# Kernel tuning notes

Hardware: AMD Instinct MI355X
Metric: run time of the kernel (lower is better)

## Reference

```python
import jax, jax.numpy as jnp
import numpy as np

HIGH_THRESHOLD = 0.1
EPS = 1e-6


def _gaussian_kernel_2d(ksize=5, sigma=1.0):
    x = np.arange(ksize, dtype=np.float32) - ksize // 2
    g = np.exp(-(x * x) / (2.0 * sigma * sigma))
    g = g / g.sum()
    return (g[:, None] * g[None, :]).astype(np.float32)  # (5,5)


def _sobel_kernels():
    gx = np.array([[-1.0, 0.0, 1.0], [-2.0, 0.0, 2.0], [-1.0, 0.0, 1.0]], np.float32)
    gy = gx.T.copy()
    return np.stack([gx, gy])[:, None]  # (2,1,3,3)


def _nms_kernels():
    # kornia get_canny_nms_kernel: 8 direction kernels, center 1, -1 at neighbor
    k = np.zeros((8, 1, 3, 3), np.float32)
    k[:, 0, 1, 1] = 1.0
    offs = [(1, 2), (0, 2), (0, 1), (0, 0), (1, 0), (2, 0), (2, 1), (2, 2)]
    for i, (r, c) in enumerate(offs):
        k[i, 0, r, c] = -1.0
    return k


def _conv(x, w, pad, mode=None):
    # x: (B,Cin,H,W), w: (Cout,Cin,kh,kw)
    if mode is not None:
        x = jnp.pad(x, ((0, 0), (0, 0), (pad, pad), (pad, pad)), mode=mode)
        padding = 'VALID'
    else:
        padding = [(pad, pad), (pad, pad)]
    return jax.lax.conv_general_dilated(
        x, w, (1, 1), padding, dimension_numbers=('NCHW', 'OIHW', 'NCHW'))


def cal_edge(x):
    dt = x.dtype
    if x.shape[1] == 3:  # rgb_to_grayscale
        w = jnp.array([0.299, 0.587, 0.114], dt).reshape(1, 3, 1, 1)
        x = jnp.sum(x * w, axis=1, keepdims=True)
    # gaussian_blur2d, reflect border (kornia default)
    blurred = _conv(x, jnp.asarray(_gaussian_kernel_2d())[None, None], 2, mode='reflect')
    # spatial_gradient (sobel, replicate border)
    grads = _conv(blurred, jnp.asarray(_sobel_kernels()), 1, mode='edge')  # (B,2,H,W)
    gx, gy = grads[:, 0:1], grads[:, 1:2]
    magnitude = jnp.sqrt(gx * gx + gy * gy + EPS)  # (B,1,H,W)
    angle = jnp.arctan2(gy, gx) * (180.0 / np.pi)
    angle = jnp.round(angle / 45.0) * 45.0
    nms_mag = _conv(magnitude, jnp.asarray(_nms_kernels()), 1)  # (B,8,H,W), zero pad
    pos_idx = jnp.mod(angle / 45.0, 8.0).astype(jnp.int32)        # (B,1,H,W)
    neg_idx = jnp.mod(angle / 45.0 + 4.0, 8.0).astype(jnp.int32)
    cp = jnp.take_along_axis(nms_mag, pos_idx, axis=1)
    cn = jnp.take_along_axis(nms_mag, neg_idx, axis=1)
    is_max = jnp.minimum(cp, cn) > 0.0
    magnitude = magnitude * is_max
    # F.threshold(mag, high, 0); then F.threshold(-e, -high, -1); e = -e
    e1 = jnp.where(magnitude > HIGH_THRESHOLD, magnitude, jnp.zeros((), dt))
    edges = -jnp.where(-e1 > -HIGH_THRESHOLD, -e1, jnp.full((), -1.0, dt))
    return edges


def setup_inputs() -> dict:
    key = jax.random.key(0)
    k1, k2 = jax.random.split(key)
    shape = (8, 3, 1024, 1024)
    op = jax.random.uniform(k1, shape, jnp.float32)
    gt = jax.random.uniform(k2, shape, jnp.float32)
    return {'op': op, 'gt': gt}


def reference(op, gt):
    edge_op = cal_edge(op)
    edge_gt = cal_edge(gt)
    return jnp.mean(jnp.abs(edge_op - edge_gt))
```

## Files before the change

### kernel.cpp

```cpp
#include <hip/hip_runtime.h>

#define N 1024
#define NN (N * N)
#define STRIPS 19
#define SEGS 32
#define SEGROWS 32
#define NWAVES (STRIPS * SEGS * 8)

__device__ __forceinline__ int refl(int i) {
    if (i < 0) return -i;
    if (i >= N) return 2 * N - 2 - i;
    return i;
}

__global__ __launch_bounds__(64)
void edge_diff_kernel(const float* __restrict__ op, const float* __restrict__ gt,
                      unsigned int* __restrict__ partials)
{
    const float w0 = 0.05448868f, w1 = 0.24420134f, w2 = 0.40261996f,
                w3 = 0.24420134f, w4 = 0.05448868f;

    int b = blockIdx.x;
    int img   = b / (STRIPS * SEGS);
    int rem   = b - img * (STRIPS * SEGS);
    int strip = rem / SEGS;
    int seg   = rem - strip * SEGS;
    int lane  = threadIdx.x;

    int cb = strip * 56 - 4;
    int c  = cb + lane;
    int cR = refl(c);

    const float* A = op + (size_t)img * 3 * NN;
    const float* B = gt + (size_t)img * 3 * NN;

    const bool cz0 = (c == 0), czN = (c == N - 1);
    const bool valid = (lane >= 4) && (lane <= 59) && (c >= 0) && (c < N);

    const int iL1 = lane - 1, iL2 = lane - 2, iR1 = lane + 1, iR2 = lane + 2;

    float ha0=0,ha1=0,ha2=0,ha3=0,ha4=0;
    float bla0=0,bla1=0,bla2=0;
    float mga0=0,mga1=0,mga2=0;
    float mgla0=0,mgla1=0,mgla2=0;
    float mgra0=0,mgra1=0,mgra2=0;
    int   axa = 0;
    float hb0=0,hb1=0,hb2=0,hb3=0,hb4=0;
    float blb0=0,blb1=0,blb2=0;
    float mgb0=0,mgb1=0,mgb2=0;
    float mglb0=0,mglb1=0,mglb2=0;
    float mgrb0=0,mgrb1=0,mgrb2=0;
    int   axb = 0;

    int acc = 0;
    const int R0 = seg * SEGROWS;

#pragma unroll 4
    for (int y = R0 - 4; y <= R0 + 35; ++y) {
        int rr = refl(y);
        const float* pa = A + (size_t)rr * N + cR;
        const float* pb = B + (size_t)rr * N + cR;

        float ga = 0.299f * pa[0] + 0.587f * pa[NN] + 0.114f * pa[2 * NN];
        float gb = 0.299f * pb[0] + 0.587f * pb[NN] + 0.114f * pb[2 * NN];

        float gal2 = __shfl(ga, iL2, 64), gal1 = __shfl(ga, iL1, 64);
        float gar1 = __shfl(ga, iR1, 64), gar2 = __shfl(ga, iR2, 64);
        float gbl2 = __shfl(gb, iL2, 64), gbl1 = __shfl(gb, iL1, 64);
        float gbr1 = __shfl(gb, iR1, 64), gbr2 = __shfl(gb, iR2, 64);
        float hna = w0*gal2 + w1*gal1 + w2*ga + w3*gar1 + w4*gar2;
        float hnb = w0*gbl2 + w1*gbl1 + w2*gb + w3*gbr1 + w4*gbr2;
        ha0=ha1; ha1=ha2; ha2=ha3; ha3=ha4; ha4=hna;
        hb0=hb1; hb1=hb2; hb2=hb3; hb3=hb4; hb4=hnb;

        float bna = w0*ha0 + w1*ha1 + w2*ha2 + w3*ha3 + w4*ha4;
        float bnb = w0*hb0 + w1*hb1 + w2*hb2 + w3*hb3 + w4*hb4;
        bla0=bla1; bla1=bla2; bla2=bna;
        blb0=blb1; blb1=blb2; blb2=bnb;

        int z = y - 3;
        float Ara = (z == 0)     ? bla1 : bla0;
        float Cra = (z == N - 1) ? bla1 : bla2;
        float Arb = (z == 0)     ? blb1 : blb0;
        float Crb = (z == N - 1) ? blb1 : blb2;

        float sa = Ara + 2.f*bla1 + Cra;  float da = Cra - Ara;
        float sb = Arb + 2.f*blb1 + Crb;  float db = Crb - Arb;

        float sal = __shfl(sa, iL1, 64), sar = __shfl(sa, iR1, 64);
        float dal = __shfl(da, iL1, 64), dar = __shfl(da, iR1, 64);
        float sbl = __shfl(sb, iL1, 64), sbr = __shfl(sb, iR1, 64);
        float dbl = __shfl(db, iL1, 64), dbr = __shfl(db, iR1, 64);
        sal = cz0 ? sa : sal;  dal = cz0 ? da : dal;
        sar = czN ? sa : sar;  dar = czN ? da : dar;
        sbl = cz0 ? sb : sbl;  dbl = cz0 ? db : dbl;
        sbr = czN ? sb : sbr;  dbr = czN ? db : dbr;

        float gxa = sar - sal;            float gya = dal + 2.f*da + dar;
        float gxb = sbr - sbl;            float gyb = dbl + 2.f*db + dbr;
        float maga = sqrtf(gxa*gxa + gya*gya + 1e-6f);
        float magb = sqrtf(gxb*gxb + gyb*gyb + 1e-6f);

        float axx = fabsf(gxa), ayy = fabsf(gya);
        int cda = (ayy <= 0.41421356f * axx) ? 0
                : (ayy >= 2.41421356f * axx) ? 1
                : (((gxa > 0.f) == (gya > 0.f)) ? 2 : 3);
        float bxx = fabsf(gxb), byy = fabsf(gyb);
        int cdb = (byy <= 0.41421356f * bxx) ? 0
                : (byy >= 2.41421356f * bxx) ? 1
                : (((gxb > 0.f) == (gyb > 0.f)) ? 2 : 3);

        float mala = __shfl(maga, iL1, 64); mala = cz0 ? 0.f : mala;
        float mara = __shfl(maga, iR1, 64); mara = czN ? 0.f : mara;
        float malb = __shfl(magb, iL1, 64); malb = cz0 ? 0.f : malb;
        float marb = __shfl(magb, iR1, 64); marb = czN ? 0.f : marb;

        mga0=mga1;   mga1=mga2;   mga2=maga;
        mgla0=mgla1; mgla1=mgla2; mgla2=mala;
        mgra0=mgra1; mgra1=mgra2; mgra2=mara;
        mgb0=mgb1;   mgb1=mgb2;   mgb2=magb;
        mglb0=mglb1; mglb1=mglb2; mglb2=malb;
        mgrb0=mgrb1; mgrb1=mgrb2; mgrb2=marb;

        int axUa = axa; axa = cda;
        int axUb = axb; axb = cdb;

        if (y >= R0 + 4) {
            int w = y - 4;
            float m0a = mga0, l0a = mgla0, r0a = mgra0;
            float m2a = mga2, l2a = mgla2, r2a = mgra2;
            float m0b = mgb0, l0b = mglb0, r0b = mgrb0;
            float m2b = mgb2, l2b = mglb2, r2b = mgrb2;
            if (w == 0)     { m0a=0; l0a=0; r0a=0; m0b=0; l0b=0; r0b=0; }
            if (w == N - 1) { m2a=0; l2a=0; r2a=0; m2b=0; l2b=0; r2b=0; }

            float n1a = (axUa == 0) ? mgra1 : (axUa == 1) ? m0a : (axUa == 2) ? r0a : l0a;
            float n2a = (axUa == 0) ? mgla1 : (axUa == 1) ? m2a : (axUa == 2) ? l2a : r2a;
            float n1b = (axUb == 0) ? mgrb1 : (axUb == 1) ? m0b : (axUb == 2) ? r0b : l0b;
            float n2b = (axUb == 0) ? mglb1 : (axUb == 1) ? m2b : (axUb == 2) ? l2b : r2b;

            bool ea = (mga1 > n1a) && (mga1 > n2a) && (mga1 > 0.1f);
            bool eb = (mgb1 > n1b) && (mgb1 > n2b) && (mgb1 > 0.1f);
            acc += (int)(valid && (ea != eb));
        }
    }

    for (int off = 32; off > 0; off >>= 1)
        acc += __shfl_down(acc, off, 64);
    if (lane == 0)
        partials[b] = (unsigned int)acc;
}

__global__ __launch_bounds__(256)
void finalize_kernel(const unsigned int* __restrict__ partials, float* __restrict__ out)
{
    __shared__ unsigned int ws[4];
    int tid = threadIdx.x;
    unsigned int sum = 0;
    for (int i = tid; i < NWAVES; i += 256)
        sum += partials[i];
    int d = (int)sum;
    for (int off = 32; off > 0; off >>= 1)
        d += __shfl_down(d, off, 64);
    if ((tid & 63) == 0) ws[tid >> 6] = (unsigned int)d;
    __syncthreads();
    if (tid == 0)
        out[0] = (float)(ws[0] + ws[1] + ws[2] + ws[3]) / 8388608.0f;
}

extern "C" void kernel_launch(void* const* d_in, const int* in_sizes, int n_in,
                              void* d_out, int out_size, void* d_ws, size_t ws_size,
                              hipStream_t stream)
{
    const float* op = (const float*)d_in[0];
    const float* gt = (const float*)d_in[1];
    unsigned int* partials = (unsigned int*)d_ws;

    edge_diff_kernel<<<dim3(NWAVES), dim3(64), 0, stream>>>(op, gt, partials);
    finalize_kernel<<<1, dim3(256), 0, stream>>>(partials, (float*)d_out);
}
```

Baseline: 232.9 us.

## Process two columns per lane with float2 loads and specialize edge strips

Each lane now handles two adjacent columns, so a wave covers 120 valid columns instead of 56. This cuts the redundant halo loads and the shuffles needed per output pixel, and interior strips use vectorized float2 loads. Border handling is moved into a templated variant that only the edge strips run. Segments are shortened to 16 rows, which gives more waves but a larger share of vertical halo rows recomputed per segment, and each lane needs more registers.

```diff
diff --git a/kernel.cpp b/kernel.cpp
--- a/kernel.cpp
+++ b/kernel.cpp
@@ -2,9 +2,9 @@
 
 #define N 1024
 #define NN (N * N)
-#define STRIPS 19
-#define SEGS 32
-#define SEGROWS 32
+#define STRIPS 9
+#define SEGS 64
+#define SEGROWS 16
 #define NWAVES (STRIPS * SEGS * 8)
 
 __device__ __forceinline__ int refl(int i) {
@@ -12,14 +12,181 @@
     if (i >= N) return 2 * N - 2 - i;
     return i;
 }
+__device__ __forceinline__ float shl(float v, int sl) { return __shfl(v, sl, 64); }
+
+struct F2 { float x, y; };
+
+__device__ __forceinline__ int axcode(float gx, float gy) {
+    float ax = fabsf(gx), ay = fabsf(gy);
+    return (ay <= 0.41421356f * ax) ? 0
+         : (ay >= 2.41421356f * ax) ? 1
+         : (((gx > 0.f) == (gy > 0.f)) ? 2 : 3);
+}
+
+__device__ __forceinline__ float pick(int code, float r, float u, float ur, float ul) {
+    return code == 0 ? r : code == 1 ? u : code == 2 ? ur : ul;
+}
+
+template<bool EC>
+__device__ __forceinline__ int strip_body(const float* __restrict__ A,
+                                          const float* __restrict__ B,
+                                          int cb, int R0, int lane)
+{
+    const float w0 = 0.05448868f, w1 = 0.24420134f, w2 = 0.40261996f,
+                w3 = 0.24420134f, w4 = 0.05448868f;
+    const int c0 = cb + 2 * lane, c1 = c0 + 1;
+    const int lm = lane - 1, lp = lane + 1;
+    const int cR0 = refl(c0), cR1 = refl(c1);
+    const bool p0 = (c0 == 0);
+    const bool pN = (c1 == N - 1);
+    const bool v0 = (lane >= 2 && lane <= 61 && c0 >= 0 && c0 < N);
+    const bool v1 = (lane >= 2 && lane <= 61 && c1 < N);
+
+    F2 ha0{},ha1{},ha2{},ha3{},ha4{}, hb0{},hb1{},hb2{},hb3{},hb4{};
+    F2 bla0{},bla1{},bla2{}, blb0{},blb1{},blb2{};
+    F2 mga0{},mga1{},mga2{}, mgla0{},mgla1{},mgla2{}, mgra0{},mgra1{},mgra2{};
+    F2 mgb0{},mgb1{},mgb2{}, mglb0{},mglb1{},mglb2{}, mgrb0{},mgrb1{},mgrb2{};
+    int axax = 0, axay = 0, axbx = 0, axby = 0;
+
+    int acc = 0;
+
+#pragma unroll 4
+    for (int y = R0 - 4; y <= R0 + SEGROWS + 3; ++y) {
+        const int rr = refl(y);
+        F2 ga, gb;
+        if (EC) {
+            const float* pa0 = A + (size_t)rr * N + cR0;
+            const float* pa1 = A + (size_t)rr * N + cR1;
+            const float* pb0 = B + (size_t)rr * N + cR0;
+            const float* pb1 = B + (size_t)rr * N + cR1;
+            ga.x = 0.299f*pa0[0] + 0.587f*pa0[NN] + 0.114f*pa0[2*NN];
+            ga.y = 0.299f*pa1[0] + 0.587f*pa1[NN] + 0.114f*pa1[2*NN];
+            gb.x = 0.299f*pb0[0] + 0.587f*pb0[NN] + 0.114f*pb0[2*NN];
+            gb.y = 0.299f*pb1[0] + 0.587f*pb1[NN] + 0.114f*pb1[2*NN];
+        } else {
+            const float* pa = A + (size_t)rr * N + c0;
+            const float* pb = B + (size_t)rr * N + c0;
+            float2 r  = *(const float2*)pa;
+            float2 g  = *(const float2*)(pa + NN);
+            float2 bb = *(const float2*)(pa + 2 * NN);
+            ga.x = 0.299f*r.x + 0.587f*g.x + 0.114f*bb.x;
+            ga.y = 0.299f*r.y + 0.587f*g.y + 0.114f*bb.y;
+            r  = *(const float2*)pb;
+            g  = *(const float2*)(pb + NN);
+            bb = *(const float2*)(pb + 2 * NN);
+            gb.x = 0.299f*r.x + 0.587f*g.x + 0.114f*bb.x;
+            gb.y = 0.299f*r.y + 0.587f*g.y + 0.114f*bb.y;
+        }
+
+        float gaLx = shl(ga.x, lm), gaLy = shl(ga.y, lm);
+        float gaRx = shl(ga.x, lp), gaRy = shl(ga.y, lp);
+        float gbLx = shl(gb.x, lm), gbLy = shl(gb.y, lm);
+        float gbRx = shl(gb.x, lp), gbRy = shl(gb.y, lp);
+        F2 hna, hnb;
+        hna.x = w0*gaLx + w1*gaLy + w2*ga.x + w3*ga.y + w4*gaRx;
+        hna.y = w0*gaLy + w1*ga.x + w2*ga.y + w3*gaRx + w4*gaRy;
+        hnb.x = w0*gbLx + w1*gbLy + w2*gb.x + w3*gb.y + w4*gbRx;
+        hnb.y = w0*gbLy + w1*gb.x + w2*gb.y + w3*gbRx + w4*gbRy;
+        ha0=ha1; ha1=ha2; ha2=ha3; ha3=ha4; ha4=hna;
+        hb0=hb1; hb1=hb2; hb2=hb3; hb3=hb4; hb4=hnb;
+
+        F2 bna, bnb;
+        bna.x = w0*ha0.x + w1*ha1.x + w2*ha2.x + w3*ha3.x + w4*ha4.x;
+        bna.y = w0*ha0.y + w1*ha1.y + w2*ha2.y + w3*ha3.y + w4*ha4.y;
+        bnb.x = w0*hb0.x + w1*hb1.x + w2*hb2.x + w3*hb3.x + w4*hb4.x;
+        bnb.y = w0*hb0.y + w1*hb1.y + w2*hb2.y + w3*hb3.y + w4*hb4.y;
+        bla0=bla1; bla1=bla2; bla2=bna;
+        blb0=blb1; blb1=blb2; blb2=bnb;
+
+        const int z = y - 3;
+        F2 bA0 = bla0, bA2 = bla2, bB0 = blb0, bB2 = blb2;
+        if (z == 0)     { bA0 = bla1; bB0 = blb1; }
+        if (z == N - 1) { bA2 = bla1; bB2 = blb1; }
+        F2 sa, da, sb, db;
+        sa.x = bA0.x + 2.f*bla1.x + bA2.x;  sa.y = bA0.y + 2.f*bla1.y + bA2.y;
+        da.x = bA2.x - bA0.x;               da.y = bA2.y - bA0.y;
+        sb.x = bB0.x + 2.f*blb1.x + bB2.x;  sb.y = bB0.y + 2.f*blb1.y + bB2.y;
+        db.x = bB2.x - bB0.x;               db.y = bB2.y - bB0.y;
+
+        float saLy = shl(sa.y, lm), saRx = shl(sa.x, lp);
+        float daLy = shl(da.y, lm), daRx = shl(da.x, lp);
+        float sbLy = shl(sb.y, lm), sbRx = shl(sb.x, lp);
+        float dbLy = shl(db.y, lm), dbRx = shl(db.x, lp);
+        if (EC) {
+            saLy = p0 ? sa.x : saLy;  daLy = p0 ? da.x : daLy;
+            sbLy = p0 ? sb.x : sbLy;  dbLy = p0 ? db.x : dbLy;
+            saRx = pN ? sa.y : saRx;  daRx = pN ? da.y : daRx;
+            sbRx = pN ? sb.y : sbRx;  dbRx = pN ? db.y : dbRx;
+        }
+        F2 gxa, gya, gxb, gyb;
+        gxa.x = sa.y - saLy;              gxa.y = saRx - sa.x;
+        gya.x = daLy + 2.f*da.x + da.y;   gya.y = da.x + 2.f*da.y + daRx;
+        gxb.x = sb.y - sbLy;              gxb.y = sbRx - sb.x;
+        gyb.x = dbLy + 2.f*db.x + db.y;   gyb.y = db.x + 2.f*db.y + dbRx;
+
+        F2 maga, magb;
+        maga.x = sqrtf(gxa.x*gxa.x + gya.x*gya.x + 1e-6f);
+        maga.y = sqrtf(gxa.y*gxa.y + gya.y*gya.y + 1e-6f);
+        magb.x = sqrtf(gxb.x*gxb.x + gyb.x*gyb.x + 1e-6f);
+        magb.y = sqrtf(gxb.y*gxb.y + gyb.y*gyb.y + 1e-6f);
+
+        int cax = axcode(gxa.x, gya.x), cay = axcode(gxa.y, gya.y);
+        int cbx = axcode(gxb.x, gyb.x), cby = axcode(gxb.y, gyb.y);
+
+        float maLy = shl(maga.y, lm), maRx = shl(maga.x, lp);
+        float mbLy = shl(magb.y, lm), mbRx = shl(magb.x, lp);
+        if (EC) {
+            maLy = p0 ? 0.f : maLy;  mbLy = p0 ? 0.f : mbLy;
+            maRx = pN ? 0.f : maRx;  mbRx = pN ? 0.f : mbRx;
+        }
+        F2 mla{maLy, maga.x}, mra{maga.y, maRx};
+        F2 mlb{mbLy, magb.x}, mrb{magb.y, mbRx};
+
+        mga0=mga1;   mga1=mga2;   mga2=maga;
+        mgla0=mgla1; mgla1=mgla2; mgla2=mla;
+        mgra0=mgra1; mgra1=mgra2; mgra2=mra;
+        mgb0=mgb1;   mgb1=mgb2;   mgb2=magb;
+        mglb0=mglb1; mglb1=mglb2; mglb2=mlb;
+        mgrb0=mgrb1; mgrb1=mgrb2; mgrb2=mrb;
+
+        const int axUax = axax, axUay = axay, axUbx = axbx, axUby = axby;
+        axax = cax; axay = cay; axbx = cbx; axby = cby;
+
+        if (y >= R0 + 4) {
+            const int w = y - 4;
+            F2 upA=mga0, upLA=mgla0, upRA=mgra0, dnA=mga2, dnLA=mgla2, dnRA=mgra2;
+            F2 upB=mgb0, upLB=mglb0, upRB=mgrb0, dnB=mgb2, dnLB=mglb2, dnRB=mgrb2;
+            if (w == 0) {
+                upA = F2{0,0}; upLA = F2{0,0}; upRA = F2{0,0};
+                upB = F2{0,0}; upLB = F2{0,0}; upRB = F2{0,0};
+            }
+            if (w == N - 1) {
+                dnA = F2{0,0}; dnLA = F2{0,0}; dnRA = F2{0,0};
+                dnB = F2{0,0}; dnLB = F2{0,0}; dnRB = F2{0,0};
+            }
+            float n1ax = pick(axUax, mgra1.x, upA.x, upRA.x, upLA.x);
+            float n2ax = pick(axUax, mgla1.x, dnA.x, dnLA.x, dnRA.x);
+            float n1ay = pick(axUay, mgra1.y, upA.y, upRA.y, upLA.y);
+            float n2ay = pick(axUay, mgla1.y, dnA.y, dnLA.y, dnRA.y);
+            float n1bx = pick(axUbx, mgrb1.x, upB.x, upRB.x, upLB.x);
+            float n2bx = pick(axUbx, mglb1.x, dnB.x, dnLB.x, dnRB.x);
+            float n1by = pick(axUby, mgrb1.y, upB.y, upRB.y, upLB.y);
+            float n2by = pick(axUby, mglb1.y, dnB.y, dnLB.y, dnRB.y);
+            bool eax = (mga1.x > n1ax) && (mga1.x > n2ax) && (mga1.x > 0.1f);
+            bool eay = (mga1.y > n1ay) && (mga1.y > n2ay) && (mga1.y > 0.1f);
+            bool ebx = (mgb1.x > n1bx) && (mgb1.x > n2bx) && (mgb1.x > 0.1f);
+            bool eby = (mgb1.y > n1by) && (mgb1.y > n2by) && (mgb1.y > 0.1f);
+            acc += (int)(v0 && (eax != ebx));
+            acc += (int)(v1 && (eay != eby));
+        }
+    }
+    return acc;
+}
 
 __global__ __launch_bounds__(64)
 void edge_diff_kernel(const float* __restrict__ op, const float* __restrict__ gt,
                       unsigned int* __restrict__ partials)
 {
-    const float w0 = 0.05448868f, w1 = 0.24420134f, w2 = 0.40261996f,
-                w3 = 0.24420134f, w4 = 0.05448868f;
-
     int b = blockIdx.x;
     int img   = b / (STRIPS * SEGS);
     int rem   = b - img * (STRIPS * SEGS);
@@ -27,128 +194,20 @@
     int seg   = rem - strip * SEGS;
     int lane  = threadIdx.x;
 
-    int cb = strip * 56 - 4;
-    int c  = cb + lane;
-    int cR = refl(c);
-
+    int cb = strip * 120 - 4;
+    int R0 = seg * SEGROWS;
     const float* A = op + (size_t)img * 3 * NN;
     const float* B = gt + (size_t)img * 3 * NN;
 
-    const bool cz0 = (c == 0), czN = (c == N - 1);
-    const bool valid = (lane >= 4) && (lane <= 59) && (c >= 0) && (c < N);
-
-    const int iL1 = lane - 1, iL2 = lane - 2, iR1 = lane + 1, iR2 = lane + 2;
-
-    float ha0=0,ha1=0,ha2=0,ha3=0,ha4=0;
-    float bla0=0,bla1=0,bla2=0;
-    float mga0=0,mga1=0,mga2=0;
-    float mgla0=0,mgla1=0,mgla2=0;
-    float mgra0=0,mgra1=0,mgra2=0;
-    int   axa = 0;
-    float hb0=0,hb1=0,hb2=0,hb3=0,hb4=0;
-    float blb0=0,blb1=0,blb2=0;
-    float mgb0=0,mgb1=0,mgb2=0;
-    float mglb0=0,mglb1=0,mglb2=0;
-    float mgrb0=0,mgrb1=0,mgrb2=0;
-    int   axb = 0;
-
-    int acc = 0;
-    const int R0 = seg * SEGROWS;
-
-#pragma unroll 4
-    for (int y = R0 - 4; y <= R0 + 35; ++y) {
-        int rr = refl(y);
-        const float* pa = A + (size_t)rr * N + cR;
-        const float* pb = B + (size_t)rr * N + cR;
-
-        float ga = 0.299f * pa[0] + 0.587f * pa[NN] + 0.114f * pa[2 * NN];
-        float gb = 0.299f * pb[0] + 0.587f * pb[NN] + 0.114f * pb[2 * NN];
-
-        float gal2 = __shfl(ga, iL2, 64), gal1 = __shfl(ga, iL1, 64);
-        float gar1 = __shfl(ga, iR1, 64), gar2 = __shfl(ga, iR2, 64);
-        float gbl2 = __shfl(gb, iL2, 64), gbl1 = __shfl(gb, iL1, 64);
-        float gbr1 = __shfl(gb, iR1, 64), gbr2 = __shfl(gb, iR2, 64);
-        float hna = w0*gal2 + w1*gal1 + w2*ga + w3*gar1 + w4*gar2;
-        float hnb = w0*gbl2 + w1*gbl1 + w2*gb + w3*gbr1 + w4*gbr2;
-        ha0=ha1; ha1=ha2; ha2=ha3; ha3=ha4; ha4=hna;
-        hb0=hb1; hb1=hb2; hb2=hb3; hb3=hb4; hb4=hnb;
-
-        float bna = w0*ha0 + w1*ha1 + w2*ha2 + w3*ha3 + w4*ha4;
-        float bnb = w0*hb0 + w1*hb1 + w2*hb2 + w3*hb3 + w4*hb4;
-        bla0=bla1; bla1=bla2; bla2=bna;
-        blb0=blb1; blb1=blb2; blb2=bnb;
-
-        int z = y - 3;
-        float Ara = (z == 0)     ? bla1 : bla0;
-        float Cra = (z == N - 1) ? bla1 : bla2;
-        float Arb = (z == 0)     ? blb1 : blb0;
-        float Crb = (z == N - 1) ? blb1 : blb2;
-
-        float sa = Ara + 2.f*bla1 + Cra;  float da = Cra - Ara;
-        float sb = Arb + 2.f*blb1 + Crb;  float db = Crb - Arb;
-
-        float sal = __shfl(sa, iL1, 64), sar = __shfl(sa, iR1, 64);
-        float dal = __shfl(da, iL1, 64), dar = __shfl(da, iR1, 64);
-        float sbl = __shfl(sb, iL1, 64), sbr = __shfl(sb, iR1, 64);
-        float dbl = __shfl(db, iL1, 64), dbr = __shfl(db, iR1, 64);
-        sal = cz0 ? sa : sal;  dal = cz0 ? da : dal;
-        sar = czN ? sa : sar;  dar = czN ? da : dar;
-        sbl = cz0 ? sb : sbl;  dbl = cz0 ? db : dbl;
-        sbr = czN ? sb : sbr;  dbr = czN ? db : dbr;
-
-        float gxa = sar - sal;            float gya = dal + 2.f*da + dar;
-        float gxb = sbr - sbl;            float gyb = dbl + 2.f*db + dbr;
-        float maga = sqrtf(gxa*gxa + gya*gya + 1e-6f);
-        float magb = sqrtf(gxb*gxb + gyb*gyb + 1e-6f);
-
-        float axx = fabsf(gxa), ayy = fabsf(gya);
-        int cda = (ayy <= 0.41421356f * axx) ? 0
-                : (ayy >= 2.41421356f * axx) ? 1
-                : (((gxa > 0.f) == (gya > 0.f)) ? 2 : 3);
-        float bxx = fabsf(gxb), byy = fabsf(gyb);
-        int cdb = (byy <= 0.41421356f * bxx) ? 0
-                : (byy >= 2.41421356f * bxx) ? 1
-                : (((gxb > 0.f) == (gyb > 0.f)) ? 2 : 3);
-
-        float mala = __shfl(maga, iL1, 64); mala = cz0 ? 0.f : mala;
-        float mara = __shfl(maga, iR1, 64); mara = czN ? 0.f : mara;
-        float malb = __shfl(magb, iL1, 64); malb = cz0 ? 0.f : malb;
-        float marb = __shfl(magb, iR1, 64); marb = czN ? 0.f : marb;
-
-        mga0=mga1;   mga1=mga2;   mga2=maga;
-        mgla0=mgla1; mgla1=mgla2; mgla2=mala;
-        mgra0=mgra1; mgra1=mgra2; mgra2=mara;
-        mgb0=mgb1;   mgb1=mgb2;   mgb2=magb;
-        mglb0=mglb1; mglb1=mglb2; mglb2=malb;
-        mgrb0=mgrb1; mgrb1=mgrb2; mgrb2=marb;
-
-        int axUa = axa; axa = cda;
-        int axUb = axb; axb = cdb;
-
-        if (y >= R0 + 4) {
-            int w = y - 4;
-            float m0a = mga0, l0a = mgla0, r0a = mgra0;
-            float m2a = mga2, l2a = mgla2, r2a = mgra2;
-            float m0b = mgb0, l0b = mglb0, r0b = mgrb0;
-            float m2b = mgb2, l2b = mglb2, r2b = mgrb2;
-            if (w == 0)     { m0a=0; l0a=0; r0a=0; m0b=0; l0b=0; r0b=0; }
-            if (w == N - 1) { m2a=0; l2a=0; r2a=0; m2b=0; l2b=0; r2b=0; }
-
-            float n1a = (axUa == 0) ? mgra1 : (axUa == 1) ? m0a : (axUa == 2) ? r0a : l0a;
-            float n2a = (axUa == 0) ? mgla1 : (axUa == 1) ? m2a : (axUa == 2) ? l2a : r2a;
-            float n1b = (axUb == 0) ? mgrb1 : (axUb == 1) ? m0b : (axUb == 2) ? r0b : l0b;
-            float n2b = (axUb == 0) ? mglb1 : (axUb == 1) ? m2b : (axUb == 2) ? l2b : r2b;
-
-            bool ea = (mga1 > n1a) && (mga1 > n2a) && (mga1 > 0.1f);
-            bool eb = (mgb1 > n1b) && (mgb1 > n2b) && (mgb1 > 0.1f);
-            acc += (int)(valid && (ea != eb));
-        }
-    }
+    int acc;
+    if (strip == 0 || strip == STRIPS - 1)
+        acc = strip_body<true>(A, B, cb, R0, lane);
+    else
+        acc = strip_body<false>(A, B, cb, R0, lane);
 
     for (int off = 32; off > 0; off >>= 1)
         acc += __shfl_down(acc, off, 64);
-    if (lane == 0)
-        partials[b] = (unsigned int)acc;
+    if (lane == 0) partials[b] = (unsigned int)acc;
 }
 
 __global__ __launch_bounds__(256)
```

New measurement: 246.2 us. +5.7%, slower.
